# Optimization experiments

Hardware: AMD Instinct MI355X
Metric: run time of the kernel (lower is better)

Reference implementation:

```python
import jax, jax.numpy as jnp
import numpy as np

N_NODES = 50000
N_EDGES = 800000
D_MODEL = 128
N_LAYERS = 3


def setup_inputs() -> dict:
    key = jax.random.key(0)
    k1, k2, k3 = jax.random.split(key, 3)
    in_feat = jax.random.normal(k1, (N_NODES, D_MODEL), dtype=jnp.float32)
    edge_index = jax.random.randint(k2, (2, N_EDGES), 0, N_NODES, dtype=jnp.int64)
    # per-layer GraphConv weights (Glorot-ish scale) and biases
    Ws = jax.random.normal(k3, (N_LAYERS, D_MODEL, D_MODEL), dtype=jnp.float32) / np.sqrt(D_MODEL)
    bs = jnp.zeros((N_LAYERS, D_MODEL), dtype=jnp.float32)
    return {"in_feat": in_feat, "edge_index": edge_index, "Ws": Ws, "bs": bs}


def _degrees(edge_index, num_nodes):
    src, dst = edge_index[0], edge_index[1]
    ones = jnp.ones(src.shape[0], dtype=jnp.float32)
    out_deg = jax.ops.segment_sum(ones, src, num_segments=num_nodes)
    in_deg = jax.ops.segment_sum(ones, dst, num_segments=num_nodes)
    # DGL GraphConv norm='both': deg^{-1/2}, clamp zero-degree to 1
    out_norm = jax.lax.rsqrt(jnp.maximum(out_deg, 1.0))
    in_norm = jax.lax.rsqrt(jnp.maximum(in_deg, 1.0))
    return out_norm, in_norm


def reference(in_feat, edge_index, Ws, bs):
    src, dst = edge_index[0], edge_index[1]
    num_nodes = in_feat.shape[0]
    out_norm, in_norm = _degrees(edge_index, num_nodes)

    h = in_feat
    for i in range(N_LAYERS):
        # symmetric normalization: D_out^{-1/2} on source side
        hs = h * out_norm[:, None]
        # gather messages along edges and sum-aggregate into destinations
        msgs = hs[src]                                   # [E, d]
        agg = jax.ops.segment_sum(msgs, dst, num_segments=num_nodes)  # [N, d]
        agg = agg * in_norm[:, None]                     # D_in^{-1/2} on dest side
        h = agg @ Ws[i] + bs[i]
    return h
```

## Files before the change

### kernel.cpp

```cpp
#include <hip/hip_runtime.h>


#define NN 50000
#define NE 800000
#define DM 128
#define NB 196
#define NGB 12500
#define CHN 12500
#define NCOP 32
#define NFB 782

typedef unsigned short u16;

#define FMA4(av, sv, wv) \
  av.x += (sv) * (wv).x; av.y += (sv) * (wv).y; av.z += (sv) * (wv).z; av.w += (sv) * (wv).w;

__device__ __forceinline__ float bf2f(u16 u) {
  return __uint_as_float((unsigned)u << 16);
}
__device__ __forceinline__ u16 f2bf(float f) {
  unsigned x = __float_as_uint(f);
  return (u16)((x + 0x7fffu + ((x >> 16) & 1u)) >> 16);
}

__global__ void k_hist(const int* __restrict__ src, const int* __restrict__ dst,
                       int* __restrict__ hcop) {
  __shared__ int h[CHN];
  int b = blockIdx.x;
  int arr   = b >> 7;
  int chunk = (b >> 5) & 3;
  int copy  = b & 31;
  const int* idx = arr ? dst : src;
  int lo = chunk * CHN;
  for (int i = threadIdx.x; i < CHN; i += 256) h[i] = 0;
  __syncthreads();
  const int4* e4 = reinterpret_cast<const int4*>(idx) + copy * (NE / 4 / NCOP);
  for (int i = threadIdx.x; i < NE / 4 / NCOP; i += 256) {
    int4 v = e4[i];
    unsigned a;
    a = (unsigned)(v.x - lo); if (a < (unsigned)CHN) atomicAdd(&h[a], 1);
    a = (unsigned)(v.y - lo); if (a < (unsigned)CHN) atomicAdd(&h[a], 1);
    a = (unsigned)(v.z - lo); if (a < (unsigned)CHN) atomicAdd(&h[a], 1);
    a = (unsigned)(v.w - lo); if (a < (unsigned)CHN) atomicAdd(&h[a], 1);
  }
  __syncthreads();
  int* o = hcop + (size_t)b * CHN;
  for (int i = threadIdx.x; i < CHN; i += 256) o[i] = h[i];
}

__global__ void k_scan_part(const int* __restrict__ hcop, int* __restrict__ co,
                            int* __restrict__ ci, int* __restrict__ bsum) {
  __shared__ int s[256];
  int i = blockIdx.x * 256 + threadIdx.x;
  int sco = 0, sci = 0;
  if (i < NN) {
    int ch = i / CHN;
    int loc = i - ch * CHN;
    const int* pco = hcop + (size_t)(ch * 32) * CHN + loc;
    const int* pci = hcop + (size_t)(128 + ch * 32) * CHN + loc;
#pragma unroll
    for (int p = 0; p < NCOP; ++p) {
      sco += pco[(size_t)p * CHN];
      sci += pci[(size_t)p * CHN];
    }
    co[i] = sco;
    ci[i] = sci;
  }
  s[threadIdx.x] = sci;
  __syncthreads();
  for (int off = 128; off > 0; off >>= 1) {
    if (threadIdx.x < off) s[threadIdx.x] += s[threadIdx.x + off];
    __syncthreads();
  }
  if (threadIdx.x == 0) bsum[blockIdx.x] = s[0];
}

__global__ void k_scan_mid(const int* __restrict__ bsum, int* __restrict__ boff,
                           int* __restrict__ rowptr) {
  __shared__ int s[256];
  int t = threadIdx.x;
  int v = (t < NB) ? bsum[t] : 0;
  s[t] = v;
  __syncthreads();
  for (int off = 1; off < 256; off <<= 1) {
    int u = (t >= off) ? s[t - off] : 0;
    __syncthreads();
    s[t] += u;
    __syncthreads();
  }
  if (t < NB) boff[t] = s[t] - v;
  if (t == 0) rowptr[NN] = NE;
}

__global__ void k_scan_out(const int* __restrict__ ci, const int* __restrict__ co,
                           const int* __restrict__ boff, int* __restrict__ rowptr,
                           float* __restrict__ onorm, float* __restrict__ inorm) {
  __shared__ int s[256];
  int t = threadIdx.x;
  int i = blockIdx.x * 256 + t;
  int v = (i < NN) ? ci[i] : 0;
  s[t] = v;
  __syncthreads();
  for (int off = 1; off < 256; off <<= 1) {
    int u = (t >= off) ? s[t - off] : 0;
    __syncthreads();
    s[t] += u;
    __syncthreads();
  }
  if (i < NN) {
    int ex = boff[blockIdx.x] + s[t] - v;
    rowptr[i] = ex;
    onorm[i] = rsqrtf(fmaxf((float)co[i], 1.0f));
    inorm[i] = rsqrtf(fmaxf((float)v, 1.0f));
  }
}

__global__ void k_pcur(const int* __restrict__ hcop_dst, const int* __restrict__ rowptr,
                       int* __restrict__ pcur) {
  int i = blockIdx.x * 256 + threadIdx.x;
  if (i >= NN) return;
  int ch = i / CHN;
  int loc = i - ch * CHN;
  int run = rowptr[i];
  const int* hb = hcop_dst + (size_t)(ch * 32) * CHN + loc;
  int* pb = pcur + (size_t)(ch * 32) * CHN + loc;
#pragma unroll
  for (int p = 0; p < NCOP; ++p) {
    pb[(size_t)p * CHN] = run;
    run += hb[(size_t)p * CHN];
  }
}

__global__ void k_fill2(const int* __restrict__ src, const int* __restrict__ dst,
                        const int* __restrict__ pcur, int* __restrict__ col,
                        const float* __restrict__ feat, u16* __restrict__ featb) {
  __shared__ int cur[CHN];
  int b = blockIdx.x;
  if (b >= 128) {
    size_t base = ((size_t)(b - 128) * 256 + threadIdx.x) * 8;
    const size_t stride = (size_t)NFB * 256 * 8;
#pragma unroll
    for (int it = 0; it < 4; ++it, base += stride) {
      if (base < (size_t)NN * DM) {
        float4 f0 = *reinterpret_cast<const float4*>(feat + base);
        float4 f1 = *reinterpret_cast<const float4*>(feat + base + 4);
        ushort4 u0 = make_ushort4(f2bf(f0.x), f2bf(f0.y), f2bf(f0.z), f2bf(f0.w));
        ushort4 u1 = make_ushort4(f2bf(f1.x), f2bf(f1.y), f2bf(f1.z), f2bf(f1.w));
        *reinterpret_cast<ushort4*>(featb + base) = u0;
        *reinterpret_cast<ushort4*>(featb + base + 4) = u1;
      }
    }
    return;
  }
  int chunk = b >> 5;
  int copy  = b & 31;
  int lo = chunk * CHN;
  const int* pc = pcur + (size_t)b * CHN;
  for (int i = threadIdx.x; i < CHN; i += 256) cur[i] = pc[i];
  __syncthreads();
  const int4* s4 = reinterpret_cast<const int4*>(src) + copy * (NE / 4 / NCOP);
  const int4* d4 = reinterpret_cast<const int4*>(dst) + copy * (NE / 4 / NCOP);
  for (int i = threadIdx.x; i < NE / 4 / NCOP; i += 256) {
    int4 s = s4[i];
    int4 d = d4[i];
    unsigned a;
    int p;
    a = (unsigned)(d.x - lo); if (a < (unsigned)CHN) { p = atomicAdd(&cur[a], 1); col[p] = s.x; }
    a = (unsigned)(d.y - lo); if (a < (unsigned)CHN) { p = atomicAdd(&cur[a], 1); col[p] = s.y; }
    a = (unsigned)(d.z - lo); if (a < (unsigned)CHN) { p = atomicAdd(&cur[a], 1); col[p] = s.z; }
    a = (unsigned)(d.w - lo); if (a < (unsigned)CHN) { p = atomicAdd(&cur[a], 1); col[p] = s.w; }
  }
}

template <int VMODE, int EXTRA, int OUTBF>
__global__ void k_gather_t(const u16* __restrict__ h, const int* __restrict__ rowptr,
                           const int* __restrict__ col, const float* __restrict__ onorm,
                           const float* __restrict__ inorm, const float* __restrict__ vin,
                           u16* __restrict__ aggb, float* __restrict__ aggf,
                           float* __restrict__ vout,
                           const float* __restrict__ mA, const float* __restrict__ mB,
                           float* __restrict__ mC,
                           const float* __restrict__ vb1, const float* __restrict__ vB1,
                           float* __restrict__ vc1,
                           const float* __restrict__ vb2, const float* __restrict__ vB2,
                           float* __restrict__ vc2) {
  if (EXTRA) {
    int eb = (int)blockIdx.x - NGB;
    if (eb >= 0) {
      if (eb < 64) {
        int i0 = eb * 2 + (threadIdx.x >> 7);
        int j = threadIdx.x & 127;
        float acc = 0.f;
        for (int k = 0; k < DM; ++k) acc += mA[i0 * DM + k] * mB[k * DM + j];
        mC[i0 * DM + j] = acc;
      } else if (EXTRA == 2) {
        int t = threadIdx.x;
        if (t < DM) {
          float acc = 0.f;
          for (int k = 0; k < DM; ++k) acc += vb1[k] * vB1[k * DM + t];
          vc1[t] = acc;
        } else {
          int j = t - DM;
          float acc = 0.f;
          for (int k = 0; k < DM; ++k) acc += vb2[k] * vB2[k * DM + j];
          vc2[j] = acc;
        }
      }
      return;
    }
  }
  int tid = blockIdx.x * blockDim.x + threadIdx.x;
  int n = tid >> 6;
  if (n >= NN) return;
  int lane = threadIdx.x & 63;
  int half = lane >> 5;
  int l32 = lane & 31;
  int beg = rowptr[n], end = rowptr[n + 1];
  const ushort4* h4 = reinterpret_cast<const ushort4*>(h);
  float4 a0 = make_float4(0.f, 0.f, 0.f, 0.f);
  float4 a1 = make_float4(0.f, 0.f, 0.f, 0.f);
  float av = 0.f;
  int e = beg + half;
  for (; e + 2 < end; e += 4) {
    int s0 = col[e], s1 = col[e + 2];
    float n0 = onorm[s0], n1 = onorm[s1];
    ushort4 u0 = h4[(size_t)s0 * 32 + l32];
    ushort4 u1 = h4[(size_t)s1 * 32 + l32];
    float4 v0 = make_float4(bf2f(u0.x), bf2f(u0.y), bf2f(u0.z), bf2f(u0.w));
    float4 v1 = make_float4(bf2f(u1.x), bf2f(u1.y), bf2f(u1.z), bf2f(u1.w));
    if (VMODE == 1) av += n0 + n1;
    if (VMODE == 2) av += n0 * vin[s0] + n1 * vin[s1];
    FMA4(a0, n0, v0)
    FMA4(a1, n1, v1)
  }
  if (e < end) {
    int s0 = col[e];
    float n0 = onorm[s0];
    ushort4 u0 = h4[(size_t)s0 * 32 + l32];
    float4 v0 = make_float4(bf2f(u0.x), bf2f(u0.y), bf2f(u0.z), bf2f(u0.w));
    if (VMODE == 1) av += n0;
    if (VMODE == 2) av += n0 * vin[s0];
    FMA4(a0, n0, v0)
  }
  a0.x += a1.x; a0.y += a1.y; a0.z += a1.z; a0.w += a1.w;
  a0.x += __shfl_xor(a0.x, 32);
  a0.y += __shfl_xor(a0.y, 32);
  a0.z += __shfl_xor(a0.z, 32);
  a0.w += __shfl_xor(a0.w, 32);
  if (VMODE) av += __shfl_xor(av, 32);
  if (half == 0) {
    float sc = inorm[n];
    float4 o = make_float4(a0.x * sc, a0.y * sc, a0.z * sc, a0.w * sc);
    if (OUTBF) {
      reinterpret_cast<ushort4*>(aggb)[(size_t)n * 32 + l32] =
          make_ushort4(f2bf(o.x), f2bf(o.y), f2bf(o.z), f2bf(o.w));
    } else {
      reinterpret_cast<float4*>(aggf)[(size_t)n * 32 + l32] = o;
    }
    if (VMODE && l32 == 0) vout[n] = av * sc;
  }
}

__launch_bounds__(256, 2)
__global__ void k_gemm_f(const float* __restrict__ x, const float* __restrict__ W,
                         const float* __restrict__ c1, const float* __restrict__ c2,
                         const float* __restrict__ c3, const float* __restrict__ v1,
                         const float* __restrict__ v2, float* __restrict__ out) {
  __shared__ float Wl[DM * 64];
  __shared__ float xs[64 * 132];

  int jhalf = blockIdx.x & 1;
  int grp   = blockIdx.x >> 1;
  int jbase = jhalf * 64;
  int rbase = grp * 64;

  {
    const float4* W4 = reinterpret_cast<const float4*>(W);
    float4* Wl4 = reinterpret_cast<float4*>(Wl);
    for (int i = threadIdx.x; i < DM * 16; i += 256) {
      int k = i >> 4, j4 = i & 15;
      Wl4[k * 16 + j4] = W4[k * 32 + jhalf * 16 + j4];
    }
    const float4* xg = reinterpret_cast<const float4*>(x) + (size_t)rbase * 32;
    float4* xs4 = reinterpret_cast<float4*>(xs);
    int lim = (NN - rbase) * 32;
    for (int i = threadIdx.x; i < 2048; i += 256) {
      int r = i >> 5, seg = i & 31;
      float4 v = (i < lim) ? xg[i] : make_float4(0.f, 0.f, 0.f, 0.f);
      xs4[r * 33 + seg] = v;
    }
  }
  __syncthreads();

  int slot = threadIdx.x >> 4;
  int lane = threadIdx.x & 15;
  int jc = lane * 4;
  float4 e1 = *reinterpret_cast<const float4*>(&c1[jbase + jc]);
  float4 e2 = *reinterpret_cast<const float4*>(&c2[jbase + jc]);
  float4 e3 = *reinterpret_cast<const float4*>(&c3[jbase + jc]);

  int r0 = rbase + slot * 4;
  int rc0 = (r0 < NN) ? r0 : NN - 1;
  int rc1 = (r0 + 1 < NN) ? r0 + 1 : NN - 1;
  int rc2 = (r0 + 2 < NN) ? r0 + 2 : NN - 1;
  int rc3 = (r0 + 3 < NN) ? r0 + 3 : NN - 1;
  const float* x0 = &xs[(slot * 4 + 0) * 132];
  const float* x1 = &xs[(slot * 4 + 1) * 132];
  const float* x2 = &xs[(slot * 4 + 2) * 132];
  const float* x3 = &xs[(slot * 4 + 3) * 132];

  float4 a0, a1, a2, a3;
  {
    float q1, q2;
    q1 = v1[rc0]; q2 = v2[rc0];
    a0.x = q2 * e1.x + q1 * e2.x + e3.x; a0.y = q2 * e1.y + q1 * e2.y + e3.y;
    a0.z = q2 * e1.z + q1 * e2.z + e3.z; a0.w = q2 * e1.w + q1 * e2.w + e3.w;
    q1 = v1[rc1]; q2 = v2[rc1];
    a1.x = q2 * e1.x + q1 * e2.x + e3.x; a1.y = q2 * e1.y + q1 * e2.y + e3.y;
    a1.z = q2 * e1.z + q1 * e2.z + e3.z; a1.w = q2 * e1.w + q1 * e2.w + e3.w;
    q1 = v1[rc2]; q2 = v2[rc2];
    a2.x = q2 * e1.x + q1 * e2.x + e3.x; a2.y = q2 * e1.y + q1 * e2.y + e3.y;
    a2.z = q2 * e1.z + q1 * e2.z + e3.z; a2.w = q2 * e1.w + q1 * e2.w + e3.w;
    q1 = v1[rc3]; q2 = v2[rc3];
    a3.x = q2 * e1.x + q1 * e2.x + e3.x; a3.y = q2 * e1.y + q1 * e2.y + e3.y;
    a3.z = q2 * e1.z + q1 * e2.z + e3.z; a3.w = q2 * e1.w + q1 * e2.w + e3.w;
  }

#pragma unroll 4
  for (int k4 = 0; k4 < DM; k4 += 4) {
    float4 xv0 = *reinterpret_cast<const float4*>(&x0[k4]);
    float4 xv1 = *reinterpret_cast<const float4*>(&x1[k4]);
    float4 xv2 = *reinterpret_cast<const float4*>(&x2[k4]);
    float4 xv3 = *reinterpret_cast<const float4*>(&x3[k4]);
    float4 w0 = *reinterpret_cast<const float4*>(&Wl[(k4 + 0) * 64 + jc]);
    float4 w1 = *reinterpret_cast<const float4*>(&Wl[(k4 + 1) * 64 + jc]);
    float4 w2 = *reinterpret_cast<const float4*>(&Wl[(k4 + 2) * 64 + jc]);
    float4 w3 = *reinterpret_cast<const float4*>(&Wl[(k4 + 3) * 64 + jc]);
    FMA4(a0, xv0.x, w0) FMA4(a0, xv0.y, w1) FMA4(a0, xv0.z, w2) FMA4(a0, xv0.w, w3)
    FMA4(a1, xv1.x, w0) FMA4(a1, xv1.y, w1) FMA4(a1, xv1.z, w2) FMA4(a1, xv1.w, w3)
    FMA4(a2, xv2.x, w0) FMA4(a2, xv2.y, w1) FMA4(a2, xv2.z, w2) FMA4(a2, xv2.w, w3)
    FMA4(a3, xv3.x, w0) FMA4(a3, xv3.y, w1) FMA4(a3, xv3.z, w2) FMA4(a3, xv3.w, w3)
  }

  float* o = out + (size_t)r0 * DM + jbase + jc;
  if (r0 + 3 < NN) {
    *reinterpret_cast<float4*>(o)          = a0;
    *reinterpret_cast<float4*>(o + DM)     = a1;
    *reinterpret_cast<float4*>(o + 2 * DM) = a2;
    *reinterpret_cast<float4*>(o + 3 * DM) = a3;
  } else {
    if (r0 + 0 < NN) *reinterpret_cast<float4*>(o)          = a0;
    if (r0 + 1 < NN) *reinterpret_cast<float4*>(o + DM)     = a1;
    if (r0 + 2 < NN) *reinterpret_cast<float4*>(o + 2 * DM) = a2;
  }
}

extern "C" void kernel_launch(void* const* d_in, const int* in_sizes, int n_in,
                              void* d_out, int out_size, void* d_ws, size_t ws_size,
                              hipStream_t stream) {
  const float* in_feat = (const float*)d_in[0];
  const int*   ei      = (const int*)d_in[1];
  const float* Ws      = (const float*)d_in[2];
  const float* bs      = (const float*)d_in[3];
  float* out = (float*)d_out;

  const int* src = ei;
  const int* dst = ei + NE;
  const float* W1 = Ws;
  const float* W2 = Ws + DM * DM;
  const float* W3 = Ws + 2 * DM * DM;
  const float* b1 = bs;
  const float* b2 = bs + DM;
  const float* b3 = bs + 2 * DM;

  char* w = (char*)d_ws;
  int* hcop   = (int*)w;            w += (size_t)256 * CHN * sizeof(int);
  int* co     = (int*)w;            w += NN * sizeof(int);
  int* ci     = (int*)w;            w += NN * sizeof(int);
  int* rowptr = (int*)w;            w += (NN + 1) * sizeof(int);
  int* bsum   = (int*)w;            w += NB * sizeof(int);
  int* boff   = (int*)w;            w += NB * sizeof(int);
  int* col    = (int*)w;            w += NE * sizeof(int);
  float* onorm = (float*)w;         w += NN * sizeof(float);
  float* inorm = (float*)w;         w += NN * sizeof(float);
  float* v1    = (float*)w;         w += NN * sizeof(float);
  float* v2    = (float*)w;         w += NN * sizeof(float);
  float* W23   = (float*)w;         w += DM * DM * sizeof(float);
  float* W123  = (float*)w;         w += DM * DM * sizeof(float);
  float* c1    = (float*)w;         w += DM * sizeof(float);
  float* c2    = (float*)w;         w += DM * sizeof(float);
  u16* featb  = (u16*)w;            w += (size_t)NN * DM * sizeof(u16);
  u16* g1b    = (u16*)w;            w += (size_t)NN * DM * sizeof(u16);
  u16* g2b    = (u16*)w;            w += (size_t)NN * DM * sizeof(u16);
  float* bufA  = (float*)w;         w += (size_t)NN * DM * sizeof(float);

  int* pcur = hcop;
  const int* hcop_dst = hcop + (size_t)128 * CHN;

  k_hist<<<256, 256, 0, stream>>>(src, dst, hcop);
  k_scan_part<<<NB, 256, 0, stream>>>(hcop, co, ci, bsum);
  k_scan_mid<<<1, 256, 0, stream>>>(bsum, boff, rowptr);
  k_scan_out<<<NB, 256, 0, stream>>>(ci, co, boff, rowptr, onorm, inorm);
  k_pcur<<<NB, 256, 0, stream>>>(hcop_dst, rowptr, pcur);
  k_fill2<<<128 + NFB, 256, 0, stream>>>(src, dst, pcur, col, in_feat, featb);

  k_gather_t<1, 1, 1><<<NGB + 64, 256, 0, stream>>>(featb, rowptr, col, onorm, inorm,
                                                    nullptr, g1b, nullptr, v1,
                                                    W2, W3, W23,
                                                    nullptr, nullptr, nullptr,
                                                    nullptr, nullptr, nullptr);
  k_gather_t<2, 2, 1><<<NGB + 65, 256, 0, stream>>>(g1b, rowptr, col, onorm, inorm,
                                                    v1, g2b, nullptr, v2,
                                                    W1, W23, W123,
                                                    b1, W23, c1, b2, W3, c2);
  k_gather_t<0, 0, 0><<<NGB, 256, 0, stream>>>(g2b, rowptr, col, onorm, inorm,
                                               nullptr, nullptr, bufA, nullptr,
                                               nullptr, nullptr, nullptr,
                                               nullptr, nullptr, nullptr,
                                               nullptr, nullptr, nullptr);

  k_gemm_f<<<1564, 256, 0, stream>>>(bufA, W123, c1, c2, b3, v1, v2, out);
}
```

Before: 228.4 us.

## Move combined weight GEMM before last aggregation using bf16 MFMA, fuse epilogue

The fp32 FMA GEMM on the aggregated layer-3 output is replaced by a bf16 MFMA GEMM that runs on the layer-2 result before the last gather. The final gather then aggregates the transformed bf16 features and adds the bias and v1/v2 correction terms directly into the output, which removes the fp32 intermediate buffer. The gather loop is unrolled to four edges per half-wave, and the scan-mid, scan-out and pcur kernels are merged into one launch. The cost is that the combined weight is rounded to bf16 and the transformed features are stored in bf16, so precision drops.

```diff
diff --git a/kernel.cpp b/kernel.cpp
--- a/kernel.cpp
+++ b/kernel.cpp
@@ -11,6 +11,8 @@
 #define NFB 782
 
 typedef unsigned short u16;
+typedef __attribute__((ext_vector_type(8))) short bf16x8;
+typedef __attribute__((ext_vector_type(4))) float f32x4;
 
 #define FMA4(av, sv, wv) \
   av.x += (sv) * (wv).x; av.y += (sv) * (wv).y; av.z += (sv) * (wv).z; av.w += (sv) * (wv).w;
@@ -21,6 +23,9 @@
 __device__ __forceinline__ u16 f2bf(float f) {
   unsigned x = __float_as_uint(f);
   return (u16)((x + 0x7fffu + ((x >> 16) & 1u)) >> 16);
+}
+__device__ __forceinline__ float4 bf4(ushort4 u) {
+  return make_float4(bf2f(u.x), bf2f(u.y), bf2f(u.z), bf2f(u.w));
 }
 
 __global__ void k_hist(const int* __restrict__ src, const int* __restrict__ dst,
@@ -75,12 +80,14 @@
   if (threadIdx.x == 0) bsum[blockIdx.x] = s[0];
 }
 
-__global__ void k_scan_mid(const int* __restrict__ bsum, int* __restrict__ boff,
-                           int* __restrict__ rowptr) {
+__global__ void k_scan_out2(const int* __restrict__ ci, const int* __restrict__ co,
+                            const int* __restrict__ bsum, int* __restrict__ rowptr,
+                            float* __restrict__ onorm, float* __restrict__ inorm,
+                            const int* __restrict__ hcop_dst, int* __restrict__ pcur) {
   __shared__ int s[256];
   int t = threadIdx.x;
-  int v = (t < NB) ? bsum[t] : 0;
-  s[t] = v;
+  int bv = (t < NB) ? bsum[t] : 0;
+  s[t] = bv;
   __syncthreads();
   for (int off = 1; off < 256; off <<= 1) {
     int u = (t >= off) ? s[t - off] : 0;
@@ -88,15 +95,9 @@
     s[t] += u;
     __syncthreads();
   }
-  if (t < NB) boff[t] = s[t] - v;
-  if (t == 0) rowptr[NN] = NE;
-}
-
-__global__ void k_scan_out(const int* __restrict__ ci, const int* __restrict__ co,
-                           const int* __restrict__ boff, int* __restrict__ rowptr,
-                           float* __restrict__ onorm, float* __restrict__ inorm) {
-  __shared__ int s[256];
-  int t = threadIdx.x;
+  int boff_blk = s[blockIdx.x] - bsum[blockIdx.x];
+  __syncthreads();
+
   int i = blockIdx.x * 256 + t;
   int v = (i < NN) ? ci[i] : 0;
   s[t] = v;
@@ -108,27 +109,22 @@
     __syncthreads();
   }
   if (i < NN) {
-    int ex = boff[blockIdx.x] + s[t] - v;
+    int ex = boff_blk + s[t] - v;
     rowptr[i] = ex;
     onorm[i] = rsqrtf(fmaxf((float)co[i], 1.0f));
     inorm[i] = rsqrtf(fmaxf((float)v, 1.0f));
-  }
-}
-
-__global__ void k_pcur(const int* __restrict__ hcop_dst, const int* __restrict__ rowptr,
-                       int* __restrict__ pcur) {
-  int i = blockIdx.x * 256 + threadIdx.x;
-  if (i >= NN) return;
-  int ch = i / CHN;
-  int loc = i - ch * CHN;
-  int run = rowptr[i];
-  const int* hb = hcop_dst + (size_t)(ch * 32) * CHN + loc;
-  int* pb = pcur + (size_t)(ch * 32) * CHN + loc;
-#pragma unroll
-  for (int p = 0; p < NCOP; ++p) {
-    pb[(size_t)p * CHN] = run;
-    run += hb[(size_t)p * CHN];
-  }
+    int ch = i / CHN;
+    int loc = i - ch * CHN;
+    const int* hb = hcop_dst + (size_t)(ch * 32) * CHN + loc;
+    int* pb = pcur + (size_t)(ch * 32) * CHN + loc;
+    int run = ex;
+#pragma unroll
+    for (int p = 0; p < NCOP; ++p) {
+      pb[(size_t)p * CHN] = run;
+      run += hb[(size_t)p * CHN];
+    }
+  }
+  if (blockIdx.x == 0 && t == 0) rowptr[NN] = NE;
 }
 
 __global__ void k_fill2(const int* __restrict__ src, const int* __restrict__ dst,
@@ -172,18 +168,21 @@
   }
 }
 
-template <int VMODE, int EXTRA, int OUTBF>
+template <int VMODE, int EXTRA, int OUTMODE>
 __global__ void k_gather_t(const u16* __restrict__ h, const int* __restrict__ rowptr,
                            const int* __restrict__ col, const float* __restrict__ onorm,
                            const float* __restrict__ inorm, const float* __restrict__ vin,
-                           u16* __restrict__ aggb, float* __restrict__ aggf,
+                           u16* __restrict__ aggb, float* __restrict__ outf,
                            float* __restrict__ vout,
                            const float* __restrict__ mA, const float* __restrict__ mB,
-                           float* __restrict__ mC,
+                           float* __restrict__ mCf, u16* __restrict__ mCt,
                            const float* __restrict__ vb1, const float* __restrict__ vB1,
                            float* __restrict__ vc1,
                            const float* __restrict__ vb2, const float* __restrict__ vB2,
-                           float* __restrict__ vc2) {
+                           float* __restrict__ vc2,
+                           const float* __restrict__ pv1, const float* __restrict__ pv2,
+                           const float* __restrict__ pc1, const float* __restrict__ pc2,
+                           const float* __restrict__ pb3) {
   if (EXTRA) {
     int eb = (int)blockIdx.x - NGB;
     if (eb >= 0) {
@@ -192,7 +191,8 @@
         int j = threadIdx.x & 127;
         float acc = 0.f;
         for (int k = 0; k < DM; ++k) acc += mA[i0 * DM + k] * mB[k * DM + j];
-        mC[i0 * DM + j] = acc;
+        if (EXTRA == 1) mCf[i0 * DM + j] = acc;
+        else            mCt[j * DM + i0] = f2bf(acc);
       } else if (EXTRA == 2) {
         int t = threadIdx.x;
         if (t < DM) {
@@ -212,37 +212,42 @@
   int tid = blockIdx.x * blockDim.x + threadIdx.x;
   int n = tid >> 6;
   if (n >= NN) return;
-  int lane = threadIdx.x & 63;
-  int half = lane >> 5;
-  int l32 = lane & 31;
+  int half = (threadIdx.x >> 5) & 1;
+  int l32 = threadIdx.x & 31;
   int beg = rowptr[n], end = rowptr[n + 1];
   const ushort4* h4 = reinterpret_cast<const ushort4*>(h);
   float4 a0 = make_float4(0.f, 0.f, 0.f, 0.f);
   float4 a1 = make_float4(0.f, 0.f, 0.f, 0.f);
+  float4 a2 = make_float4(0.f, 0.f, 0.f, 0.f);
+  float4 a3 = make_float4(0.f, 0.f, 0.f, 0.f);
   float av = 0.f;
   int e = beg + half;
-  for (; e + 2 < end; e += 4) {
-    int s0 = col[e], s1 = col[e + 2];
-    float n0 = onorm[s0], n1 = onorm[s1];
-    ushort4 u0 = h4[(size_t)s0 * 32 + l32];
-    ushort4 u1 = h4[(size_t)s1 * 32 + l32];
-    float4 v0 = make_float4(bf2f(u0.x), bf2f(u0.y), bf2f(u0.z), bf2f(u0.w));
-    float4 v1 = make_float4(bf2f(u1.x), bf2f(u1.y), bf2f(u1.z), bf2f(u1.w));
-    if (VMODE == 1) av += n0 + n1;
-    if (VMODE == 2) av += n0 * vin[s0] + n1 * vin[s1];
+  for (; e + 6 < end; e += 8) {
+    int s0 = col[e], s1 = col[e + 2], s2 = col[e + 4], s3 = col[e + 6];
+    float n0 = onorm[s0], n1 = onorm[s1], n2 = onorm[s2], n3 = onorm[s3];
+    float4 v0 = bf4(h4[(size_t)s0 * 32 + l32]);
+    float4 v1 = bf4(h4[(size_t)s1 * 32 + l32]);
+    float4 v2 = bf4(h4[(size_t)s2 * 32 + l32]);
+    float4 v3 = bf4(h4[(size_t)s3 * 32 + l32]);
+    if (VMODE == 1) av += n0 + n1 + n2 + n3;
+    if (VMODE == 2) av += n0 * vin[s0] + n1 * vin[s1] + n2 * vin[s2] + n3 * vin[s3];
     FMA4(a0, n0, v0)
     FMA4(a1, n1, v1)
-  }
-  if (e < end) {
+    FMA4(a2, n2, v2)
+    FMA4(a3, n3, v3)
+  }
+  for (; e < end; e += 2) {
     int s0 = col[e];
     float n0 = onorm[s0];
-    ushort4 u0 = h4[(size_t)s0 * 32 + l32];
-    float4 v0 = make_float4(bf2f(u0.x), bf2f(u0.y), bf2f(u0.z), bf2f(u0.w));
+    float4 v0 = bf4(h4[(size_t)s0 * 32 + l32]);
     if (VMODE == 1) av += n0;
     if (VMODE == 2) av += n0 * vin[s0];
     FMA4(a0, n0, v0)
   }
-  a0.x += a1.x; a0.y += a1.y; a0.z += a1.z; a0.w += a1.w;
+  a0.x += a1.x + a2.x + a3.x;
+  a0.y += a1.y + a2.y + a3.y;
+  a0.z += a1.z + a2.z + a3.z;
+  a0.w += a1.w + a2.w + a3.w;
   a0.x += __shfl_xor(a0.x, 32);
   a0.y += __shfl_xor(a0.y, 32);
   a0.z += __shfl_xor(a0.z, 32);
@@ -251,107 +256,60 @@
   if (half == 0) {
     float sc = inorm[n];
     float4 o = make_float4(a0.x * sc, a0.y * sc, a0.z * sc, a0.w * sc);
-    if (OUTBF) {
+    if (OUTMODE == 0) {
       reinterpret_cast<ushort4*>(aggb)[(size_t)n * 32 + l32] =
           make_ushort4(f2bf(o.x), f2bf(o.y), f2bf(o.z), f2bf(o.w));
     } else {
-      reinterpret_cast<float4*>(aggf)[(size_t)n * 32 + l32] = o;
+      int jc = l32 * 4;
+      float4 e1 = *reinterpret_cast<const float4*>(pc1 + jc);
+      float4 e2 = *reinterpret_cast<const float4*>(pc2 + jc);
+      float4 e3 = *reinterpret_cast<const float4*>(pb3 + jc);
+      float q1 = pv1[n], q2 = pv2[n];
+      o.x += q2 * e1.x + q1 * e2.x + e3.x;
+      o.y += q2 * e1.y + q1 * e2.y + e3.y;
+      o.z += q2 * e1.z + q1 * e2.z + e3.z;
+      o.w += q2 * e1.w + q1 * e2.w + e3.w;
+      reinterpret_cast<float4*>(outf)[(size_t)n * 32 + l32] = o;
     }
     if (VMODE && l32 == 0) vout[n] = av * sc;
   }
 }
 
-__launch_bounds__(256, 2)
-__global__ void k_gemm_f(const float* __restrict__ x, const float* __restrict__ W,
-                         const float* __restrict__ c1, const float* __restrict__ c2,
-                         const float* __restrict__ c3, const float* __restrict__ v1,
-                         const float* __restrict__ v2, float* __restrict__ out) {
-  __shared__ float Wl[DM * 64];
-  __shared__ float xs[64 * 132];
-
-  int jhalf = blockIdx.x & 1;
-  int grp   = blockIdx.x >> 1;
-  int jbase = jhalf * 64;
-  int rbase = grp * 64;
-
-  {
-    const float4* W4 = reinterpret_cast<const float4*>(W);
-    float4* Wl4 = reinterpret_cast<float4*>(Wl);
-    for (int i = threadIdx.x; i < DM * 16; i += 256) {
-      int k = i >> 4, j4 = i & 15;
-      Wl4[k * 16 + j4] = W4[k * 32 + jhalf * 16 + j4];
-    }
-    const float4* xg = reinterpret_cast<const float4*>(x) + (size_t)rbase * 32;
-    float4* xs4 = reinterpret_cast<float4*>(xs);
-    int lim = (NN - rbase) * 32;
-    for (int i = threadIdx.x; i < 2048; i += 256) {
-      int r = i >> 5, seg = i & 31;
-      float4 v = (i < lim) ? xg[i] : make_float4(0.f, 0.f, 0.f, 0.f);
-      xs4[r * 33 + seg] = v;
-    }
-  }
-  __syncthreads();
-
-  int slot = threadIdx.x >> 4;
-  int lane = threadIdx.x & 15;
-  int jc = lane * 4;
-  float4 e1 = *reinterpret_cast<const float4*>(&c1[jbase + jc]);
-  float4 e2 = *reinterpret_cast<const float4*>(&c2[jbase + jc]);
-  float4 e3 = *reinterpret_cast<const float4*>(&c3[jbase + jc]);
-
-  int r0 = rbase + slot * 4;
-  int rc0 = (r0 < NN) ? r0 : NN - 1;
-  int rc1 = (r0 + 1 < NN) ? r0 + 1 : NN - 1;
-  int rc2 = (r0 + 2 < NN) ? r0 + 2 : NN - 1;
-  int rc3 = (r0 + 3 < NN) ? r0 + 3 : NN - 1;
-  const float* x0 = &xs[(slot * 4 + 0) * 132];
-  const float* x1 = &xs[(slot * 4 + 1) * 132];
-  const float* x2 = &xs[(slot * 4 + 2) * 132];
-  const float* x3 = &xs[(slot * 4 + 3) * 132];
-
-  float4 a0, a1, a2, a3;
-  {
-    float q1, q2;
-    q1 = v1[rc0]; q2 = v2[rc0];
-    a0.x = q2 * e1.x + q1 * e2.x + e3.x; a0.y = q2 * e1.y + q1 * e2.y + e3.y;
-    a0.z = q2 * e1.z + q1 * e2.z + e3.z; a0.w = q2 * e1.w + q1 * e2.w + e3.w;
-    q1 = v1[rc1]; q2 = v2[rc1];
-    a1.x = q2 * e1.x + q1 * e2.x + e3.x; a1.y = q2 * e1.y + q1 * e2.y + e3.y;
-    a1.z = q2 * e1.z + q1 * e2.z + e3.z; a1.w = q2 * e1.w + q1 * e2.w + e3.w;
-    q1 = v1[rc2]; q2 = v2[rc2];
-    a2.x = q2 * e1.x + q1 * e2.x + e3.x; a2.y = q2 * e1.y + q1 * e2.y + e3.y;
-    a2.z = q2 * e1.z + q1 * e2.z + e3.z; a2.w = q2 * e1.w + q1 * e2.w + e3.w;
-    q1 = v1[rc3]; q2 = v2[rc3];
-    a3.x = q2 * e1.x + q1 * e2.x + e3.x; a3.y = q2 * e1.y + q1 * e2.y + e3.y;
-    a3.z = q2 * e1.z + q1 * e2.z + e3.z; a3.w = q2 * e1.w + q1 * e2.w + e3.w;
-  }
-
-#pragma unroll 4
-  for (int k4 = 0; k4 < DM; k4 += 4) {
-    float4 xv0 = *reinterpret_cast<const float4*>(&x0[k4]);
-    float4 xv1 = *reinterpret_cast<const float4*>(&x1[k4]);
-    float4 xv2 = *reinterpret_cast<const float4*>(&x2[k4]);
-    float4 xv3 = *reinterpret_cast<const float4*>(&x3[k4]);
-    float4 w0 = *reinterpret_cast<const float4*>(&Wl[(k4 + 0) * 64 + jc]);
-    float4 w1 = *reinterpret_cast<const float4*>(&Wl[(k4 + 1) * 64 + jc]);
-    float4 w2 = *reinterpret_cast<const float4*>(&Wl[(k4 + 2) * 64 + jc]);
-    float4 w3 = *reinterpret_cast<const float4*>(&Wl[(k4 + 3) * 64 + jc]);
-    FMA4(a0, xv0.x, w0) FMA4(a0, xv0.y, w1) FMA4(a0, xv0.z, w2) FMA4(a0, xv0.w, w3)
-    FMA4(a1, xv1.x, w0) FMA4(a1, xv1.y, w1) FMA4(a1, xv1.z, w2) FMA4(a1, xv1.w, w3)
-    FMA4(a2, xv2.x, w0) FMA4(a2, xv2.y, w1) FMA4(a2, xv2.z, w2) FMA4(a2, xv2.w, w3)
-    FMA4(a3, xv3.x, w0) FMA4(a3, xv3.y, w1) FMA4(a3, xv3.z, w2) FMA4(a3, xv3.w, w3)
-  }
-
-  float* o = out + (size_t)r0 * DM + jbase + jc;
-  if (r0 + 3 < NN) {
-    *reinterpret_cast<float4*>(o)          = a0;
-    *reinterpret_cast<float4*>(o + DM)     = a1;
-    *reinterpret_cast<float4*>(o + 2 * DM) = a2;
-    *reinterpret_cast<float4*>(o + 3 * DM) = a3;
-  } else {
-    if (r0 + 0 < NN) *reinterpret_cast<float4*>(o)          = a0;
-    if (r0 + 1 < NN) *reinterpret_cast<float4*>(o + DM)     = a1;
-    if (r0 + 2 < NN) *reinterpret_cast<float4*>(o + 2 * DM) = a2;
+__launch_bounds__(256, 4)
+__global__ void k_gemm_mfma(const u16* __restrict__ A, const u16* __restrict__ Bt,
+                            u16* __restrict__ T) {
+  int w = threadIdx.x >> 6;
+  int l = threadIdx.x & 63;
+  int rbase = blockIdx.x * 32 + 16 * (w & 1);
+  int jb0   = 64 * (w >> 1);
+  int row = rbase + (l & 15);
+  int rr = row < NN ? row : NN - 1;
+  int kg = (l >> 4) * 8;
+  const short* As = reinterpret_cast<const short*>(A);
+  const short* Bs = reinterpret_cast<const short*>(Bt);
+  bf16x8 fa0 = *reinterpret_cast<const bf16x8*>(As + (size_t)rr * DM + 0 * 32 + kg);
+  bf16x8 fa1 = *reinterpret_cast<const bf16x8*>(As + (size_t)rr * DM + 1 * 32 + kg);
+  bf16x8 fa2 = *reinterpret_cast<const bf16x8*>(As + (size_t)rr * DM + 2 * 32 + kg);
+  bf16x8 fa3 = *reinterpret_cast<const bf16x8*>(As + (size_t)rr * DM + 3 * 32 + kg);
+#pragma unroll
+  for (int ct = 0; ct < 4; ++ct) {
+    int jb = jb0 + ct * 16;
+    const short* bp = Bs + (size_t)(jb + (l & 15)) * DM + kg;
+    bf16x8 fb0 = *reinterpret_cast<const bf16x8*>(bp + 0 * 32);
+    bf16x8 fb1 = *reinterpret_cast<const bf16x8*>(bp + 1 * 32);
+    bf16x8 fb2 = *reinterpret_cast<const bf16x8*>(bp + 2 * 32);
+    bf16x8 fb3 = *reinterpret_cast<const bf16x8*>(bp + 3 * 32);
+    f32x4 c = {0.f, 0.f, 0.f, 0.f};
+    c = __builtin_amdgcn_mfma_f32_16x16x32_bf16(fa0, fb0, c, 0, 0, 0);
+    c = __builtin_amdgcn_mfma_f32_16x16x32_bf16(fa1, fb1, c, 0, 0, 0);
+    c = __builtin_amdgcn_mfma_f32_16x16x32_bf16(fa2, fb2, c, 0, 0, 0);
+    c = __builtin_amdgcn_mfma_f32_16x16x32_bf16(fa3, fb3, c, 0, 0, 0);
+    int orow = rbase + (l >> 4) * 4;
+    int ocol = jb + (l & 15);
+#pragma unroll
+    for (int r = 0; r < 4; ++r) {
+      if (orow + r < NN) T[(size_t)(orow + r) * DM + ocol] = f2bf(c[r]);
+    }
   }
 }
 
@@ -379,45 +337,44 @@
   int* ci     = (int*)w;            w += NN * sizeof(int);
   int* rowptr = (int*)w;            w += (NN + 1) * sizeof(int);
   int* bsum   = (int*)w;            w += NB * sizeof(int);
-  int* boff   = (int*)w;            w += NB * sizeof(int);
   int* col    = (int*)w;            w += NE * sizeof(int);
   float* onorm = (float*)w;         w += NN * sizeof(float);
   float* inorm = (float*)w;         w += NN * sizeof(float);
   float* v1    = (float*)w;         w += NN * sizeof(float);
   float* v2    = (float*)w;         w += NN * sizeof(float);
   float* W23   = (float*)w;         w += DM * DM * sizeof(float);
-  float* W123  = (float*)w;         w += DM * DM * sizeof(float);
+  u16*   W123t = (u16*)w;           w += DM * DM * sizeof(u16);
   float* c1    = (float*)w;         w += DM * sizeof(float);
   float* c2    = (float*)w;         w += DM * sizeof(float);
   u16* featb  = (u16*)w;            w += (size_t)NN * DM * sizeof(u16);
   u16* g1b    = (u16*)w;            w += (size_t)NN * DM * sizeof(u16);
   u16* g2b    = (u16*)w;            w += (size_t)NN * DM * sizeof(u16);
-  float* bufA  = (float*)w;         w += (size_t)NN * DM * sizeof(float);
+  u16* tb     = (u16*)w;            w += (size_t)NN * DM * sizeof(u16);
 
   int* pcur = hcop;
   const int* hcop_dst = hcop + (size_t)128 * CHN;
 
   k_hist<<<256, 256, 0, stream>>>(src, dst, hcop);
   k_scan_part<<<NB, 256, 0, stream>>>(hcop, co, ci, bsum);
-  k_scan_mid<<<1, 256, 0, stream>>>(bsum, boff, rowptr);
-  k_scan_out<<<NB, 256, 0, stream>>>(ci, co, boff, rowptr, onorm, inorm);
-  k_pcur<<<NB, 256, 0, stream>>>(hcop_dst, rowptr, pcur);
+  k_scan_out2<<<NB, 256, 0, stream>>>(ci, co, bsum, rowptr, onorm, inorm, hcop_dst, pcur);
   k_fill2<<<128 + NFB, 256, 0, stream>>>(src, dst, pcur, col, in_feat, featb);
 
-  k_gather_t<1, 1, 1><<<NGB + 64, 256, 0, stream>>>(featb, rowptr, col, onorm, inorm,
+  k_gather_t<1, 1, 0><<<NGB + 64, 256, 0, stream>>>(featb, rowptr, col, onorm, inorm,
                                                     nullptr, g1b, nullptr, v1,
-                                                    W2, W3, W23,
+                                                    W2, W3, W23, nullptr,
                                                     nullptr, nullptr, nullptr,
-                                                    nullptr, nullptr, nullptr);
-  k_gather_t<2, 2, 1><<<NGB + 65, 256, 0, stream>>>(g1b, rowptr, col, onorm, inorm,
+                                                    nullptr, nullptr, nullptr,
+                                                    nullptr, nullptr, nullptr, nullptr, nullptr);
+  k_gather_t<2, 2, 0><<<NGB + 65, 256, 0, stream>>>(g1b, rowptr, col, onorm, inorm,
                                                     v1, g2b, nullptr, v2,
-                                                    W1, W23, W123,
-                                                    b1, W23, c1, b2, W3, c2);
-  k_gather_t<0, 0, 0><<<NGB, 256, 0, stream>>>(g2b, rowptr, col, onorm, inorm,
-                                               nullptr, nullptr, bufA, nullptr,
+                                                    W1, W23, nullptr, W123t,
+                                                    b1, W23, c1, b2, W3, c2,
+                                                    nullptr, nullptr, nullptr, nullptr, nullptr);
+  k_gemm_mfma<<<(NN + 31) / 32, 256, 0, stream>>>(g2b, W123t, tb);
+  k_gather_t<0, 0, 1><<<NGB, 256, 0, stream>>>(tb, rowptr, col, onorm, inorm,
+                                               nullptr, nullptr, out, nullptr,
+                                               nullptr, nullptr, nullptr, nullptr,
                                                nullptr, nullptr, nullptr,
                                                nullptr, nullptr, nullptr,
-                                               nullptr, nullptr, nullptr);
-
-  k_gemm_f<<<1564, 256, 0, stream>>>(bufA, W123, c1, c2, b3, v1, v2, out);
-}
+                                               v1, v2, c1, c2, b3);
+}
```

After: 204.0 us. -10.7%, faster.
